# Performance work log

Measured on AMD Instinct MI355X. Metric: run time of the kernel, lower is better.

Reference implementation:

```python
import jax, jax.numpy as jnp
import numpy as np
import math

# dims
B, T, HFEAT, E = 32, 8, 128, 128
NUM_CLS, NUM_GLOBAL = 4, 2
NSP = NUM_CLS + NUM_GLOBAL            # 6 special tokens
SCALES = (1, 4, 8)
WINDOW = 4
NHEAD = 8
DH = E // NHEAD                        # 16
NLAYERS = 2                            # blocks per scale = ceil(6/3)
NS = len(SCALES)
F = 512                                # dim_feedforward
ROPE_BASE = 100000.0
NEG = -1e9


def setup_inputs() -> dict:
    key = jax.random.key(0)
    ks = jax.random.split(key, 16)
    def rn(k, shape, s=0.02):
        return jax.random.normal(k, shape, jnp.float32) * s
    inp = {
        'embeddings': jax.random.normal(ks[0], (B, T, NSP + HFEAT, E), jnp.float32),
        'cls_tokens': rn(ks[1], (NUM_CLS, E)),
        'global_tokens': rn(ks[2], (NUM_GLOBAL, E)),
        'Wq': rn(ks[3], (NS, NLAYERS, E, E)),
        'bq': jnp.zeros((NS, NLAYERS, E), jnp.float32),
        'Wk': rn(ks[4], (NS, NLAYERS, E, E)),
        'bk': jnp.zeros((NS, NLAYERS, E), jnp.float32),
        'Wv': rn(ks[5], (NS, NLAYERS, E, E)),
        'bv': jnp.zeros((NS, NLAYERS, E), jnp.float32),
        'Wo': rn(ks[6], (NS, NLAYERS, E, E)),
        'bo': jnp.zeros((NS, NLAYERS, E), jnp.float32),
        'ln1_g': jnp.ones((NS, NLAYERS, E), jnp.float32),
        'ln1_b': jnp.zeros((NS, NLAYERS, E), jnp.float32),
        'ln2_g': jnp.ones((NS, NLAYERS, E), jnp.float32),
        'ln2_b': jnp.zeros((NS, NLAYERS, E), jnp.float32),
        'W1': rn(ks[7], (NS, NLAYERS, E, F)),
        'b1': jnp.zeros((NS, NLAYERS, F), jnp.float32),
        'W2': rn(ks[8], (NS, NLAYERS, F, E)),
        'b2': jnp.zeros((NS, NLAYERS, E), jnp.float32),
        'out_g': jnp.ones((E,), jnp.float32),
        'out_b': jnp.zeros((E,), jnp.float32),
    }
    return inp


def _layernorm(x, g, b, eps=1e-5):
    mu = x.mean(-1, keepdims=True)
    var = ((x - mu) ** 2).mean(-1, keepdims=True)
    return (x - mu) * jax.lax.rsqrt(var + eps) * g + b


def _rope(x):
    # x: (BT, L, H, DH); rotate-half RoPE over head dim
    L = x.shape[1]
    half = DH // 2
    inv = ROPE_BASE ** (-jnp.arange(half, dtype=jnp.float32) / half)
    ang = jnp.arange(L, dtype=jnp.float32)[:, None] * inv[None, :]   # (L, half)
    cos = jnp.cos(ang)[None, :, None, :]
    sin = jnp.sin(ang)[None, :, None, :]
    x1, x2 = x[..., :half], x[..., half:]
    return jnp.concatenate([x1 * cos - x2 * sin, x1 * sin + x2 * cos], axis=-1)


def _sparse_bias(L):
    # global(first NSP) rows/cols fully connected, others window +-WINDOW, diag allowed
    i = jnp.arange(L)
    allowed = (jnp.abs(i[:, None] - i[None, :]) <= WINDOW) | (i[:, None] < NSP) | (i[None, :] < NSP)
    return jnp.where(allowed, 0.0, NEG).astype(jnp.float32)  # (L, L) additive


def _encoder(x, s, Wq, bq, Wk, bk, Wv, bv, Wo, bo, ln1_g, ln1_b, ln2_g, ln2_b, W1, b1, W2, b2, bias):
    # x: (BT, L, E); pre-norm transformer encoder with RoPE attention
    BT, L, _ = x.shape
    for l in range(NLAYERS):
        h = _layernorm(x, ln1_g[s, l], ln1_b[s, l])
        q = (h @ Wq[s, l] + bq[s, l]).reshape(BT, L, NHEAD, DH)
        k = (h @ Wk[s, l] + bk[s, l]).reshape(BT, L, NHEAD, DH)
        v = (h @ Wv[s, l] + bv[s, l]).reshape(BT, L, NHEAD, DH)
        q, k = _rope(q), _rope(k)
        scores = jnp.einsum('blhd,bmhd->bhlm', q, k) / math.sqrt(DH) + bias[None, None]
        attn = jax.nn.softmax(scores, axis=-1)
        o = jnp.einsum('bhlm,bmhd->blhd', attn, v).reshape(BT, L, E)
        x = x + o @ Wo[s, l] + bo[s, l]
        h2 = _layernorm(x, ln2_g[s, l], ln2_b[s, l])
        x = x + jax.nn.gelu(h2 @ W1[s, l] + b1[s, l]) @ W2[s, l] + b2[s, l]
    return x


def reference(embeddings, cls_tokens, global_tokens, Wq, bq, Wk, bk, Wv, bv, Wo, bo,
              ln1_g, ln1_b, ln2_g, ln2_b, W1, b1, W2, b2, out_g, out_b):
    Bb, Tt, HC, Ee = embeddings.shape
    feats = embeddings[..., NSP:, :]                                 # (B,T,H,E)
    specials = jnp.broadcast_to(
        jnp.concatenate([cls_tokens, global_tokens], axis=0)[None, None],
        (Bb, Tt, NSP, Ee))
    cls_per_scale = []
    for s, g in enumerate(SCALES):
        H = feats.shape[2]
        K = H // g  # H divisible by all scales
        grouped = feats.reshape(Bb, Tt, K, g, Ee).mean(axis=3)       # contiguous mean grouping
        seq = jnp.concatenate([specials, grouped], axis=2)           # (B,T,L,E)
        L = NSP + K
        x = seq.reshape(Bb * Tt, L, Ee)
        bias = _sparse_bias(L)
        out = _encoder(x, s, Wq, bq, Wk, bk, Wv, bv, Wo, bo,
                       ln1_g, ln1_b, ln2_g, ln2_b, W1, b1, W2, b2, bias)
        cls_per_scale.append(out.reshape(Bb, Tt, L, Ee)[..., :NUM_CLS, :])
    cls_out = jnp.stack(cls_per_scale, axis=0).mean(axis=0)          # (B,T,num_cls,E)
    cls_out = _layernorm(cls_out, out_g, out_b)
    return cls_out.reshape(Bb, Tt, NUM_CLS * Ee)
```

## Files before the change

### kernel.cpp

```cpp
#include <hip/hip_runtime.h>
#include <hip/hip_bf16.h>

#define BT     256
#define EDIM   128
#define NSP    6
#define RT     49664
#define O1     34304
#define O2     44032
#define KSTR   20

typedef unsigned short u16;
typedef short s16x8 __attribute__((ext_vector_type(8)));
typedef float f32x4 __attribute__((ext_vector_type(4)));

__device__ __forceinline__ float u2f(u16 u){ union{unsigned i; float f;} v; v.i=((unsigned)u)<<16; return v.f; }
__device__ __forceinline__ u16 f2u(float f){
  union{float f; unsigned i;} v; v.f = f;
  unsigned r = v.i + 0x7FFF + ((v.i >> 16) & 1);
  return (u16)(r >> 16);
}
__device__ __forceinline__ float ldin(const void* p, size_t idx, int flag){
  return flag ? u2f(((const u16*)p)[idx]) : ((const float*)p)[idx];
}
__device__ __forceinline__ void unp8(uint4 v, float* f){
  f[0]=u2f((u16)(v.x)); f[1]=u2f((u16)(v.x>>16));
  f[2]=u2f((u16)(v.y)); f[3]=u2f((u16)(v.y>>16));
  f[4]=u2f((u16)(v.z)); f[5]=u2f((u16)(v.z>>16));
  f[6]=u2f((u16)(v.w)); f[7]=u2f((u16)(v.w>>16));
}

__device__ __forceinline__ void rowinfo(int row, int& s, int& r, int& L, int& g){
  if (row < O1){ s=0; r=row;    L=134; g=1; }
  else if (row < O2){ s=1; r=row-O1; L=38; g=4; }
  else { s=2; r=row-O2; L=22; g=8; }
}

__device__ __forceinline__ float gelu_f(float x){
  float t = tanhf(0.7978845608f*(x + 0.044715f*x*x*x));
  return 0.5f*x*(1.f+t);
}

__global__ void detect_k(const void* ln1g, int* flagp){
  unsigned v = *(const unsigned*)ln1g;
  *flagp = (v == 0x3F803F80u) ? 1 : 0;
}

struct CArg { const void* src; unsigned dstoff; unsigned n; unsigned inblk; unsigned outblk; };
struct CArgs { CArg a[12]; };
__global__ __launch_bounds__(256) void conv_k(CArgs ca, u16* stage, const int* flagp){
  int i = blockIdx.y;
  int flag = *flagp;
  const CArg& c = ca.a[i];
  for (unsigned idx = blockIdx.x*256u + threadIdx.x; idx < c.n; idx += gridDim.x*256u){
    unsigned blk = idx / c.inblk, r = idx % c.inblk;
    float v = flag ? u2f(((const u16*)c.src)[idx]) : ((const float*)c.src)[idx];
    stage[c.dstoff + blk*c.outblk + r] = flag ? ((const u16*)c.src)[idx] : f2u(v);
  }
}

__global__ __launch_bounds__(256) void convw_k(const void* s0, const void* s1, const void* s2,
                                               u16* dst, int K, int N, int Nsrc, const int* flagp)
{
  int flag = *flagp;
  const void* srcs[3] = {s0, s1, s2};
  int total = 6 * K * N;
  for (int idx = blockIdx.x*256 + threadIdx.x; idx < total; idx += gridDim.x*256) {
    int blk = idx / (K*N);
    int rem = idx % (K*N);
    int j = rem & 7;
    int t = rem >> 3;
    int n = t % N;
    int ck = t / N;
    int k = ck*8 + j;
    int w = n / Nsrc;
    int nn = n - w*Nsrc;
    size_t sidx = (size_t)blk*K*Nsrc + (size_t)k*Nsrc + nn;
    dst[idx] = flag ? ((const u16*)srcs[w])[sidx] : f2u(((const float*)srcs[w])[sidx]);
  }
}

__global__ __launch_bounds__(128) void build_k(const void* __restrict__ emb,
                                               const void* __restrict__ cls,
                                               const void* __restrict__ glob,
                                               float* __restrict__ x,
                                               u16* __restrict__ H,
                                               const u16* __restrict__ lnG,
                                               const u16* __restrict__ lnB,
                                               const int* flagp)
{
  __shared__ float red[4];
  int flag = *flagp;
  int row = blockIdx.x, e = threadIdx.x;
  int s, r, L, g; rowinfo(row, s, r, L, g);
  int seq = r / L, pos = r % L;
  float val;
  if (pos < NSP) {
    val = (pos < 4) ? ldin(cls, pos*EDIM + e, flag) : ldin(glob, (pos-4)*EDIM + e, flag);
  } else {
    int k = pos - NSP;
    size_t base = ((size_t)seq*134 + NSP + (size_t)k*g)*EDIM + e;
    float sum = 0.f;
    for (int j = 0; j < g; j++) sum += ldin(emb, base + (size_t)j*EDIM, flag);
    val = sum / (float)g;
  }
  x[(size_t)row*EDIM + e] = val;
  int wid = e >> 6;
  float sum = val, ss = val*val;
  #pragma unroll
  for (int off = 32; off; off >>= 1) { sum += __shfl_xor(sum, off); ss += __shfl_xor(ss, off); }
  if ((e & 63) == 0) { red[wid] = sum; red[2+wid] = ss; }
  __syncthreads();
  float ts = red[0]+red[1], tss = red[2]+red[3];
  float mu = ts * (1.f/128.f);
  float var = tss * (1.f/128.f) - mu*mu;
  float rs = rsqrtf(var + 1e-5f);
  const u16* gp = lnG + s*2*EDIM;
  const u16* bp = lnB + s*2*EDIM;
  H[(size_t)row*EDIM + e] = f2u((val-mu)*rs*u2f(gp[e]) + u2f(bp[e]));
}

template<int EPI>
__global__ __launch_bounds__(256) void gemm64_k(
    const u16* __restrict__ A,
    const u16* __restrict__ Wt, const u16* __restrict__ Bias,
    u16* __restrict__ C, int ldc, int N, int layer,
    float* __restrict__ X, u16* __restrict__ H,
    const u16* __restrict__ lnG, const u16* __restrict__ lnB, int lnidx)
{
  __shared__ u16 As[4][16*136];
  __shared__ u16 Bs[16*128*8];
  const int row0 = blockIdx.x * 64;
  const int n0 = blockIdx.y * 128;
  const int s = row0 < O1 ? 0 : (row0 < O2 ? 1 : 2);
  const u16* Wp = Wt + (size_t)(s*2+layer)*128*N;
  const u16* bp = Bias + (size_t)(s*2+layer)*N + n0;
  const int tid = threadIdx.x;
  const int lane = tid & 63, w = tid >> 6;
  const int g = lane >> 4, l15 = lane & 15;

  #pragma unroll
  for (int i = 0; i < 4; i++) {
    int unit = lane + i*64;
    int r = unit >> 4, kc = unit & 15;
    *(uint4*)&As[w][r*136 + kc*8] = *(const uint4*)(A + (size_t)(row0 + w*16 + r)*128 + kc*8);
  }
  #pragma unroll
  for (int i = 0; i < 8; i++) {
    int u = tid + i*256;
    int kb = u >> 7, nn = u & 127;
    *(uint4*)&Bs[u*8] = *(const uint4*)(Wp + ((size_t)kb*N + n0 + nn)*8);
  }
  __syncthreads();

  f32x4 acc[8];
  #pragma unroll
  for (int nt = 0; nt < 8; nt++) acc[nt] = (f32x4){0.f,0.f,0.f,0.f};
  #pragma unroll
  for (int ks = 0; ks < 4; ks++) {
    int c = ks*4 + g;
    s16x8 af = *(const s16x8*)&As[w][l15*136 + c*8];
    #pragma unroll
    for (int nt = 0; nt < 8; nt++) {
      s16x8 bf = *(const s16x8*)&Bs[(c*128 + nt*16 + l15)*8];
      acc[nt] = __builtin_amdgcn_mfma_f32_16x16x32_bf16(af, bf, acc[nt], 0, 0, 0);
    }
  }

  float bb[8];
  #pragma unroll
  for (int nt = 0; nt < 8; nt++) bb[nt] = u2f(bp[nt*16 + l15]);

  if (EPI == 0) {
    #pragma unroll
    for (int reg = 0; reg < 4; reg++) {
      int row = row0 + w*16 + g*4 + reg;
      #pragma unroll
      for (int nt = 0; nt < 8; nt++)
        C[(size_t)row*ldc + n0 + nt*16 + l15] = f2u(acc[nt][reg] + bb[nt]);
    }
  } else {
    float gam[8], bet[8];
    const u16* gp = lnG + (s*2+lnidx)*EDIM;
    const u16* bpn = lnB + (s*2+lnidx)*EDIM;
    #pragma unroll
    for (int nt = 0; nt < 8; nt++) { gam[nt] = u2f(gp[nt*16+l15]); bet[nt] = u2f(bpn[nt*16+l15]); }
    #pragma unroll
    for (int reg = 0; reg < 4; reg++) {
      int row = row0 + w*16 + g*4 + reg;
      float vals[8], ps = 0.f, pss = 0.f;
      #pragma unroll
      for (int nt = 0; nt < 8; nt++) {
        size_t cidx = (size_t)row*128 + nt*16 + l15;
        float v = acc[nt][reg] + bb[nt] + X[cidx];
        vals[nt] = v; ps += v; pss += v*v;
      }
      #pragma unroll
      for (int off = 1; off < 16; off <<= 1) { ps += __shfl_xor(ps, off); pss += __shfl_xor(pss, off); }
      float mu = ps * (1.f/128.f);
      float var = pss * (1.f/128.f) - mu*mu;
      float rs = rsqrtf(var + 1e-5f);
      #pragma unroll
      for (int nt = 0; nt < 8; nt++) {
        size_t cidx = (size_t)row*128 + nt*16 + l15;
        X[cidx] = vals[nt];
        H[cidx] = f2u((vals[nt]-mu)*rs*gam[nt] + bet[nt]);
      }
    }
  }
}

template<int LNFUSE>
__global__ __launch_bounds__(256) void ffn_k(
    const u16* __restrict__ A,
    const u16* __restrict__ W1t, const u16* __restrict__ B1,
    const u16* __restrict__ W2t, const u16* __restrict__ B2,
    float* __restrict__ X,
    u16* __restrict__ H, const u16* __restrict__ lnG, const u16* __restrict__ lnB,
    int lnidx, int layer)
{
  __shared__ u16 As[4][16*136];
  __shared__ u16 Bs1[16*32*8];
  __shared__ u16 Bs2[4*128*8];
  __shared__ u16 Ts[4][16*40];
  const int row0 = blockIdx.x * 64;
  const int s = row0 < O1 ? 0 : (row0 < O2 ? 1 : 2);
  const u16* W1p = W1t + (size_t)(s*2+layer)*65536;
  const u16* b1p = B1 + (s*2+layer)*512;
  const u16* W2p = W2t + (size_t)(s*2+layer)*65536;
  const u16* b2p = B2 + (s*2+layer)*128;
  const int tid = threadIdx.x;
  const int lane = tid & 63, w = tid >> 6;
  const int g = lane >> 4, l15 = lane & 15;

  #pragma unroll
  for (int i = 0; i < 4; i++) {
    int unit = lane + i*64;
    int r = unit >> 4, kc = unit & 15;
    *(uint4*)&As[w][r*136 + kc*8] = *(const uint4*)(A + (size_t)(row0 + w*16 + r)*128 + kc*8);
  }

  f32x4 acc2[8];
  #pragma unroll
  for (int nt = 0; nt < 8; nt++) acc2[nt] = (f32x4){0.f,0.f,0.f,0.f};

  for (int f0 = 0; f0 < 512; f0 += 32) {
    __syncthreads();
    #pragma unroll
    for (int i = 0; i < 2; i++) {
      int u = tid + i*256;
      int kb = u >> 5, nn = u & 31;
      *(uint4*)&Bs1[u*8] = *(const uint4*)(W1p + ((size_t)kb*512 + f0 + nn)*8);
      *(uint4*)&Bs2[u*8] = *(const uint4*)(W2p + (size_t)f0*128 + u*8);
    }
    __syncthreads();
    f32x4 acc1[2];
    acc1[0] = (f32x4){0.f,0.f,0.f,0.f};
    acc1[1] = (f32x4){0.f,0.f,0.f,0.f};
    #pragma unroll
    for (int ks = 0; ks < 4; ks++) {
      int c = ks*4 + g;
      s16x8 af = *(const s16x8*)&As[w][l15*136 + c*8];
      #pragma unroll
      for (int nt = 0; nt < 2; nt++) {
        s16x8 bf = *(const s16x8*)&Bs1[(c*32 + nt*16 + l15)*8];
        acc1[nt] = __builtin_amdgcn_mfma_f32_16x16x32_bf16(af, bf, acc1[nt], 0, 0, 0);
      }
    }
    #pragma unroll
    for (int nt = 0; nt < 2; nt++) {
      float bb1 = u2f(b1p[f0 + nt*16 + l15]);
      #pragma unroll
      for (int reg = 0; reg < 4; reg++)
        Ts[w][(g*4+reg)*40 + nt*16 + l15] = f2u(gelu_f(acc1[nt][reg] + bb1));
    }
    int c2 = g;
    s16x8 af2 = *(const s16x8*)&Ts[w][l15*40 + c2*8];
    #pragma unroll
    for (int nt = 0; nt < 8; nt++) {
      s16x8 bf = *(const s16x8*)&Bs2[(c2*128 + nt*16 + l15)*8];
      acc2[nt] = __builtin_amdgcn_mfma_f32_16x16x32_bf16(af2, bf, acc2[nt], 0, 0, 0);
    }
  }

  float bb2[8];
  #pragma unroll
  for (int nt = 0; nt < 8; nt++) bb2[nt] = u2f(b2p[nt*16 + l15]);

  if (LNFUSE) {
    float gam[8], bet[8];
    const u16* gp = lnG + (s*2+lnidx)*EDIM;
    const u16* bpn = lnB + (s*2+lnidx)*EDIM;
    #pragma unroll
    for (int nt = 0; nt < 8; nt++) { gam[nt] = u2f(gp[nt*16+l15]); bet[nt] = u2f(bpn[nt*16+l15]); }
    #pragma unroll
    for (int reg = 0; reg < 4; reg++) {
      int row = row0 + w*16 + g*4 + reg;
      float vals[8], ps = 0.f, pss = 0.f;
      #pragma unroll
      for (int nt = 0; nt < 8; nt++) {
        size_t cidx = (size_t)row*128 + nt*16 + l15;
        float v = acc2[nt][reg] + bb2[nt] + X[cidx];
        vals[nt] = v; ps += v; pss += v*v;
      }
      #pragma unroll
      for (int off = 1; off < 16; off <<= 1) { ps += __shfl_xor(ps, off); pss += __shfl_xor(pss, off); }
      float mu = ps * (1.f/128.f);
      float var = pss * (1.f/128.f) - mu*mu;
      float rs = rsqrtf(var + 1e-5f);
      #pragma unroll
      for (int nt = 0; nt < 8; nt++) {
        size_t cidx = (size_t)row*128 + nt*16 + l15;
        X[cidx] = vals[nt];
        H[cidx] = f2u((vals[nt]-mu)*rs*gam[nt] + bet[nt]);
      }
    }
  } else {
    #pragma unroll
    for (int reg = 0; reg < 4; reg++) {
      int row = row0 + w*16 + g*4 + reg;
      #pragma unroll
      for (int nt = 0; nt < 8; nt++) {
        size_t cidx = (size_t)row*128 + nt*16 + l15;
        X[cidx] += acc2[nt][reg] + bb2[nt];
      }
    }
  }
}

__global__ __launch_bounds__(128) void attn_k(const u16* __restrict__ qkv, u16* __restrict__ o)
{
  __shared__ float Ks[134*KSTR];
  __shared__ float Vs[134*KSTR];
  int gseq = blockIdx.x, hd = blockIdx.y;
  int L, base;
  if (gseq < 256)      { L = 134; base = gseq*134; }
  else if (gseq < 512) { L = 38;  base = O1 + (gseq-256)*38; }
  else                 { L = 22;  base = O2 + (gseq-512)*22; }
  int tid = threadIdx.x;
  for (int u = tid; u < L*2; u += 128) {
    int kv = u & 1, row = u >> 1;
    const u16* p = qkv + (size_t)(base+row)*384 + 128 + kv*128 + hd*16;
    uint4 w0 = *(const uint4*)p, w1 = *(const uint4*)(p+8);
    float f[16];
    unp8(w0, f); unp8(w1, f+8);
    if (kv == 0) {
      #pragma unroll
      for (int d = 0; d < 8; d++) {
        float inv = __expf(-(float)d * (11.512925465f/8.f));
        float ang = (float)row * inv;
        float cs = __cosf(ang), sn = __sinf(ang);
        float a = f[d], b = f[d+8];
        f[d]   = a*cs - b*sn;
        f[d+8] = a*sn + b*cs;
      }
    }
    float* dst = (kv ? Vs : Ks) + row*KSTR;
    #pragma unroll
    for (int d = 0; d < 16; d++) dst[d] = f[d];
  }
  __syncthreads();

  for (int it = tid; it < L - NSP; it += 128) {
    int row = NSP + it;
    const u16* qp = qkv + (size_t)(base+row)*384 + hd*16;
    uint4 w0 = *(const uint4*)qp, w1 = *(const uint4*)(qp+8);
    float q[16]; unp8(w0, q); unp8(w1, q+8);
    #pragma unroll
    for (int d = 0; d < 8; d++) {
      float inv = __expf(-(float)d * (11.512925465f/8.f));
      float ang = (float)row * inv;
      float cs = __cosf(ang), sn = __sinf(ang);
      float a = q[d], b = q[d+8];
      q[d]   = a*cs - b*sn;
      q[d+8] = a*sn + b*cs;
    }
    float m = -1e30f, l = 0.f, oa[16] = {};
    auto step = [&](int j){
      const float4* kr = (const float4*)(Ks + j*KSTR);
      float4 k0 = kr[0], k1 = kr[1], k2 = kr[2], k3 = kr[3];
      float sc = q[0]*k0.x + q[1]*k0.y + q[2]*k0.z + q[3]*k0.w
               + q[4]*k1.x + q[5]*k1.y + q[6]*k1.z + q[7]*k1.w
               + q[8]*k2.x + q[9]*k2.y + q[10]*k2.z + q[11]*k2.w
               + q[12]*k3.x + q[13]*k3.y + q[14]*k3.z + q[15]*k3.w;
      sc *= 0.25f;
      float nm = fmaxf(m, sc);
      float scale = __expf(m - nm);
      float pexp = __expf(sc - nm);
      l = l*scale + pexp;
      const float4* vr = (const float4*)(Vs + j*KSTR);
      float4 v0 = vr[0], v1 = vr[1], v2 = vr[2], v3 = vr[3];
      oa[0]=oa[0]*scale+pexp*v0.x;  oa[1]=oa[1]*scale+pexp*v0.y;
      oa[2]=oa[2]*scale+pexp*v0.z;  oa[3]=oa[3]*scale+pexp*v0.w;
      oa[4]=oa[4]*scale+pexp*v1.x;  oa[5]=oa[5]*scale+pexp*v1.y;
      oa[6]=oa[6]*scale+pexp*v1.z;  oa[7]=oa[7]*scale+pexp*v1.w;
      oa[8]=oa[8]*scale+pexp*v2.x;  oa[9]=oa[9]*scale+pexp*v2.y;
      oa[10]=oa[10]*scale+pexp*v2.z; oa[11]=oa[11]*scale+pexp*v2.w;
      oa[12]=oa[12]*scale+pexp*v3.x; oa[13]=oa[13]*scale+pexp*v3.y;
      oa[14]=oa[14]*scale+pexp*v3.z; oa[15]=oa[15]*scale+pexp*v3.w;
      m = nm;
    };
    #pragma unroll
    for (int j = 0; j < NSP; j++) step(j);
    int jlo = (row-4 > NSP) ? row-4 : NSP;
    int jhi = (row+4 < L-1) ? row+4 : L-1;
    for (int j = jlo; j <= jhi; j++) step(j);
    float invl = 1.f/l;
    u16* op = o + (size_t)(base+row)*EDIM + hd*16;
    #pragma unroll
    for (int d = 0; d < 16; d++) op[d] = f2u(oa[d]*invl);
  }

  if (tid < 96) {
    int row = tid >> 4;
    int u = tid & 15;
    const u16* qp = qkv + (size_t)(base+row)*384 + hd*16;
    uint4 w0 = *(const uint4*)qp, w1 = *(const uint4*)(qp+8);
    float q[16]; unp8(w0, q); unp8(w1, q+8);
    #pragma unroll
    for (int d = 0; d < 8; d++) {
      float inv = __expf(-(float)d * (11.512925465f/8.f));
      float ang = (float)row * inv;
      float cs = __cosf(ang), sn = __sinf(ang);
      float a = q[d], b = q[d+8];
      q[d]   = a*cs - b*sn;
      q[d+8] = a*sn + b*cs;
    }
    float m = -1e30f, l = 0.f, oa[16] = {};
    for (int j = u; j < L; j += 16) {
      const float4* kr = (const float4*)(Ks + j*KSTR);
      float4 k0 = kr[0], k1 = kr[1], k2 = kr[2], k3 = kr[3];
      float sc = q[0]*k0.x + q[1]*k0.y + q[2]*k0.z + q[3]*k0.w
               + q[4]*k1.x + q[5]*k1.y + q[6]*k1.z + q[7]*k1.w
               + q[8]*k2.x + q[9]*k2.y + q[10]*k2.z + q[11]*k2.w
               + q[12]*k3.x + q[13]*k3.y + q[14]*k3.z + q[15]*k3.w;
      sc *= 0.25f;
      float nm = fmaxf(m, sc);
      float scale = __expf(m - nm);
      float pexp = __expf(sc - nm);
      l = l*scale + pexp;
      const float4* vr = (const float4*)(Vs + j*KSTR);
      float4 v0 = vr[0], v1 = vr[1], v2 = vr[2], v3 = vr[3];
      oa[0]=oa[0]*scale+pexp*v0.x;  oa[1]=oa[1]*scale+pexp*v0.y;
      oa[2]=oa[2]*scale+pexp*v0.z;  oa[3]=oa[3]*scale+pexp*v0.w;
      oa[4]=oa[4]*scale+pexp*v1.x;  oa[5]=oa[5]*scale+pexp*v1.y;
      oa[6]=oa[6]*scale+pexp*v1.z;  oa[7]=oa[7]*scale+pexp*v1.w;
      oa[8]=oa[8]*scale+pexp*v2.x;  oa[9]=oa[9]*scale+pexp*v2.y;
      oa[10]=oa[10]*scale+pexp*v2.z; oa[11]=oa[11]*scale+pexp*v2.w;
      oa[12]=oa[12]*scale+pexp*v3.x; oa[13]=oa[13]*scale+pexp*v3.y;
      oa[14]=oa[14]*scale+pexp*v3.z; oa[15]=oa[15]*scale+pexp*v3.w;
      m = nm;
    }
    #pragma unroll
    for (int off = 1; off < 16; off <<= 1) {
      float m2 = __shfl_xor(m, off);
      float l2 = __shfl_xor(l, off);
      float nm = fmaxf(m, m2);
      float s1 = __expf(m - nm), s2 = __expf(m2 - nm);
      #pragma unroll
      for (int d = 0; d < 16; d++) {
        float o2 = __shfl_xor(oa[d], off);
        oa[d] = oa[d]*s1 + o2*s2;
      }
      l = l*s1 + l2*s2;
      m = nm;
    }
    if (u == 0) {
      float invl = 1.f/l;
      u16* op = o + (size_t)(base+row)*EDIM + hd*16;
      #pragma unroll
      for (int d = 0; d < 16; d++) op[d] = f2u(oa[d]*invl);
    }
  }
}

__global__ __launch_bounds__(256) void final_k(const float* __restrict__ x,
                                               const u16* __restrict__ G,
                                               const u16* __restrict__ Bt,
                                               void* __restrict__ out, const int* flagp)
{
  int flag = *flagp;
  int wid = threadIdx.x >> 6, lane = threadIdx.x & 63;
  int idx = blockIdx.x*4 + wid;
  int seq = idx >> 2, c = idx & 3;
  size_t r0 = ((size_t)seq*134 + c)*EDIM;
  size_t r1 = ((size_t)O1 + (size_t)seq*38 + c)*EDIM;
  size_t r2 = ((size_t)O2 + (size_t)seq*22 + c)*EDIM;
  float v0 = (x[r0+lane]    + x[r1+lane]    + x[r2+lane])    * (1.f/3.f);
  float v1 = (x[r0+64+lane] + x[r1+64+lane] + x[r2+64+lane]) * (1.f/3.f);
  float sum = v0 + v1;
  #pragma unroll
  for (int off = 32; off; off >>= 1) sum += __shfl_xor(sum, off);
  float mu = sum * (1.f/128.f);
  float d0 = v0 - mu, d1 = v1 - mu;
  float var = d0*d0 + d1*d1;
  #pragma unroll
  for (int off = 32; off; off >>= 1) var += __shfl_xor(var, off);
  var *= (1.f/128.f);
  float rs = rsqrtf(var + 1e-5f);
  float o0 = d0*rs*u2f(G[lane])    + u2f(Bt[lane]);
  float o1 = d1*rs*u2f(G[64+lane]) + u2f(Bt[64+lane]);
  size_t oi0 = (size_t)seq*512 + c*128 + lane;
  if (flag) { ((u16*)out)[oi0] = f2u(o0); ((u16*)out)[oi0+64] = f2u(o1); }
  else      { ((float*)out)[oi0] = o0;    ((float*)out)[oi0+64] = o1; }
}

#define S_WQKV 0u
#define S_BQKV 294912u
#define S_WO   297216u
#define S_BO   395520u
#define S_W1   396288u
#define S_B1   789504u
#define S_W2   792576u
#define S_B2   1185792u
#define S_L1G  1186560u
#define S_L1B  1187328u
#define S_L2G  1188096u
#define S_L2B  1188864u
#define S_OG   1189632u
#define S_OB   1189760u

extern "C" void kernel_launch(void* const* d_in, const int* in_sizes, int n_in,
                              void* d_out, int out_size, void* d_ws, size_t ws_size,
                              hipStream_t stream) {
  char* wsb = (char*)d_ws;
  int*   flagp = (int*)wsb;
  u16*   stage = (u16*)(wsb + 64);
  float* x     = (float*)(wsb + (size_t)2379840);
  u16*   h     = (u16*)(wsb + (size_t)27807808);
  u16*   qkv   = (u16*)(wsb + (size_t)40521792);

  detect_k<<<1, 1, 0, stream>>>(d_in[11], flagp);

  CArgs ca;
  CArg list[12] = {
    { d_in[4],  S_BQKV,       768, 128, 384 },
    { d_in[6],  S_BQKV+128u,  768, 128, 384 },
    { d_in[8],  S_BQKV+256u,  768, 128, 384 },
    { d_in[10], S_BO,         768, 128, 128 },
    { d_in[16], S_B1,        3072, 512, 512 },
    { d_in[18], S_B2,         768, 128, 128 },
    { d_in[11], S_L1G,        768, 128, 128 },
    { d_in[12], S_L1B,        768, 128, 128 },
    { d_in[13], S_L2G,        768, 128, 128 },
    { d_in[14], S_L2B,        768, 128, 128 },
    { d_in[19], S_OG,         128, 128, 128 },
    { d_in[20], S_OB,         128, 128, 128 },
  };
  for (int i = 0; i < 12; i++) ca.a[i] = list[i];
  conv_k<<<dim3(4, 12), 256, 0, stream>>>(ca, stage, flagp);

  convw_k<<<256, 256, 0, stream>>>(d_in[3], d_in[5], d_in[7], stage+S_WQKV, 128, 384, 128, flagp);
  convw_k<<<128, 256, 0, stream>>>(d_in[9], d_in[9], d_in[9], stage+S_WO,   128, 128, 128, flagp);
  convw_k<<<256, 256, 0, stream>>>(d_in[15],d_in[15],d_in[15],stage+S_W1,   128, 512, 512, flagp);
  convw_k<<<256, 256, 0, stream>>>(d_in[17],d_in[17],d_in[17],stage+S_W2,   512, 128, 128, flagp);

  build_k<<<RT, 128, 0, stream>>>(d_in[0], d_in[1], d_in[2], x, h, stage+S_L1G, stage+S_L1B, flagp);

  for (int l = 0; l < 2; l++) {
    gemm64_k<0><<<dim3(RT/64, 3), 256, 0, stream>>>(h, stage+S_WQKV, stage+S_BQKV, qkv, 384, 384, l,
                                                    nullptr, nullptr, nullptr, nullptr, 0);
    attn_k<<<dim3(768, 8), 128, 0, stream>>>(qkv, h);
    gemm64_k<3><<<dim3(RT/64, 1), 256, 0, stream>>>(h, stage+S_WO, stage+S_BO, nullptr, 128, 128, l,
                                                    x, h, stage+S_L2G, stage+S_L2B, l);
    if (l == 0)
      ffn_k<1><<<RT/64, 256, 0, stream>>>(h, stage+S_W1, stage+S_B1, stage+S_W2, stage+S_B2, x, h, stage+S_L1G, stage+S_L1B, 1, l);
    else
      ffn_k<0><<<RT/64, 256, 0, stream>>>(h, stage+S_W1, stage+S_B1, stage+S_W2, stage+S_B2, x, nullptr, nullptr, nullptr, 0, l);
  }
  final_k<<<BT, 256, 0, stream>>>(x, stage+S_OG, stage+S_OB, d_out, flagp);
}
```

Measured before the change: 397.2 us.

## Load FFN weights directly into registers and use exp-based GELU

The FFN kernel no longer stages the activation tile and the W1/W2 weight tiles through shared memory. Each wave reads its MFMA operands straight from global memory (relying on cache) and prefetches the next W1 slice into registers, which removes the per-iteration __syncthreads barriers. GELU is rewritten as x*sigmoid(2u) using a fast exp and a hardware reciprocal instead of tanhf. The cost is higher register pressure, since the weights are no longer shared across waves and each wave fetches them separately, plus slightly different GELU rounding.

```diff
diff --git a/kernel.cpp b/kernel.cpp
--- a/kernel.cpp
+++ b/kernel.cpp
@@ -36,8 +36,8 @@
 }
 
 __device__ __forceinline__ float gelu_f(float x){
-  float t = tanhf(0.7978845608f*(x + 0.044715f*x*x*x));
-  return 0.5f*x*(1.f+t);
+  float u = x*(1.5957691216f + 0.0713548162f*x*x);
+  return x * __builtin_amdgcn_rcpf(1.f + __expf(-u));
 }
 
 __global__ void detect_k(const void* ln1g, int* flagp){
@@ -218,9 +218,6 @@
     u16* __restrict__ H, const u16* __restrict__ lnG, const u16* __restrict__ lnB,
     int lnidx, int layer)
 {
-  __shared__ u16 As[4][16*136];
-  __shared__ u16 Bs1[16*32*8];
-  __shared__ u16 Bs2[4*128*8];
   __shared__ u16 Ts[4][16*40];
   const int row0 = blockIdx.x * 64;
   const int s = row0 < O1 ? 0 : (row0 < O2 ? 1 : 2);
@@ -232,40 +229,53 @@
   const int lane = tid & 63, w = tid >> 6;
   const int g = lane >> 4, l15 = lane & 15;
 
-  #pragma unroll
-  for (int i = 0; i < 4; i++) {
-    int unit = lane + i*64;
-    int r = unit >> 4, kc = unit & 15;
-    *(uint4*)&As[w][r*136 + kc*8] = *(const uint4*)(A + (size_t)(row0 + w*16 + r)*128 + kc*8);
-  }
+  s16x8 af[4];
+  {
+    const u16* arow = A + (size_t)(row0 + w*16 + l15)*128;
+    #pragma unroll
+    for (int ks = 0; ks < 4; ks++) af[ks] = *(const s16x8*)(arow + (ks*4 + g)*8);
+  }
+
+  const u16* w1base = W1p + ((size_t)g*512 + l15)*8;
+  const u16* w2base = W2p + ((size_t)g*128 + l15)*8;
 
   f32x4 acc2[8];
   #pragma unroll
   for (int nt = 0; nt < 8; nt++) acc2[nt] = (f32x4){0.f,0.f,0.f,0.f};
 
+  s16x8 bw1[8];
+  #pragma unroll
+  for (int ks = 0; ks < 4; ks++) {
+    #pragma unroll
+    for (int nt = 0; nt < 2; nt++)
+      bw1[ks*2+nt] = *(const s16x8*)(w1base + (size_t)(ks*2048 + nt*16)*8);
+  }
+
   for (int f0 = 0; f0 < 512; f0 += 32) {
-    __syncthreads();
-    #pragma unroll
-    for (int i = 0; i < 2; i++) {
-      int u = tid + i*256;
-      int kb = u >> 5, nn = u & 31;
-      *(uint4*)&Bs1[u*8] = *(const uint4*)(W1p + ((size_t)kb*512 + f0 + nn)*8);
-      *(uint4*)&Bs2[u*8] = *(const uint4*)(W2p + (size_t)f0*128 + u*8);
-    }
-    __syncthreads();
+    s16x8 bw2[8];
+    #pragma unroll
+    for (int nt = 0; nt < 8; nt++)
+      bw2[nt] = *(const s16x8*)(w2base + (size_t)(f0*16 + nt*16)*8);
+
     f32x4 acc1[2];
     acc1[0] = (f32x4){0.f,0.f,0.f,0.f};
     acc1[1] = (f32x4){0.f,0.f,0.f,0.f};
     #pragma unroll
     for (int ks = 0; ks < 4; ks++) {
-      int c = ks*4 + g;
-      s16x8 af = *(const s16x8*)&As[w][l15*136 + c*8];
-      #pragma unroll
-      for (int nt = 0; nt < 2; nt++) {
-        s16x8 bf = *(const s16x8*)&Bs1[(c*32 + nt*16 + l15)*8];
-        acc1[nt] = __builtin_amdgcn_mfma_f32_16x16x32_bf16(af, bf, acc1[nt], 0, 0, 0);
-      }
-    }
+      acc1[0] = __builtin_amdgcn_mfma_f32_16x16x32_bf16(af[ks], bw1[ks*2+0], acc1[0], 0, 0, 0);
+      acc1[1] = __builtin_amdgcn_mfma_f32_16x16x32_bf16(af[ks], bw1[ks*2+1], acc1[1], 0, 0, 0);
+    }
+
+    {
+      int fn = (f0 + 32) & 511;
+      #pragma unroll
+      for (int ks = 0; ks < 4; ks++) {
+        #pragma unroll
+        for (int nt = 0; nt < 2; nt++)
+          bw1[ks*2+nt] = *(const s16x8*)(w1base + (size_t)(ks*2048 + fn + nt*16)*8);
+      }
+    }
+
     #pragma unroll
     for (int nt = 0; nt < 2; nt++) {
       float bb1 = u2f(b1p[f0 + nt*16 + l15]);
@@ -273,13 +283,11 @@
       for (int reg = 0; reg < 4; reg++)
         Ts[w][(g*4+reg)*40 + nt*16 + l15] = f2u(gelu_f(acc1[nt][reg] + bb1));
     }
-    int c2 = g;
-    s16x8 af2 = *(const s16x8*)&Ts[w][l15*40 + c2*8];
-    #pragma unroll
-    for (int nt = 0; nt < 8; nt++) {
-      s16x8 bf = *(const s16x8*)&Bs2[(c2*128 + nt*16 + l15)*8];
-      acc2[nt] = __builtin_amdgcn_mfma_f32_16x16x32_bf16(af2, bf, acc2[nt], 0, 0, 0);
-    }
+
+    s16x8 af2 = *(const s16x8*)&Ts[w][l15*40 + g*8];
+    #pragma unroll
+    for (int nt = 0; nt < 8; nt++)
+      acc2[nt] = __builtin_amdgcn_mfma_f32_16x16x32_bf16(af2, bw2[nt], acc2[nt], 0, 0, 0);
   }
 
   float bb2[8];
```

Measured after the change: 379.8 us. -4.4%, faster.
